# Optimization experiments

Measured on AMD Instinct MI355X. Metric: run time of the kernel, lower is better.

The kernel has to match this reference:

```python
import jax, jax.numpy as jnp
import numpy as np

N, NF, D, GH, E, B = 4096, 128, 64, 64, 32768, 32
NG, STEPS = 3, 3  # n_gcn, set2set processing steps


def setup_inputs() -> dict:
    key = jax.random.key(0)
    ks = iter(jax.random.split(key, 64))
    nrm = lambda shape: jax.random.normal(next(ks), shape, dtype=jnp.float32) * 0.05
    inp = {
        'x': jax.random.normal(next(ks), (N, NF), dtype=jnp.float32),
        'edge_attr': jax.random.uniform(next(ks), (E,), dtype=jnp.float32),
        'edge_idx': jax.random.randint(next(ks), (2, E), 0, N),
        'batch_map': jnp.sort(jax.random.randint(next(ks), (N,), 0, B)),
        # pre-GC MLP: NF->D, D->D, D->D (ReLU each)
        'pre_W0': nrm((NF, D)), 'pre_b0': nrm((D,)),
        'pre_W1': nrm((D, D)), 'pre_b1': nrm((D,)),
        'pre_W2': nrm((D, D)), 'pre_b2': nrm((D,)),
        # NNConv edge nets (stacked over NG layers): 1->GH->D*D
        'enn_W1': nrm((NG, 1, GH)), 'enn_b1': nrm((NG, GH)),
        'enn_W2': nrm((NG, GH, D * D)), 'enn_b2': nrm((NG, D * D)),
        'root_W': nrm((NG, D, D)), 'conv_b': nrm((NG, D)),
        # GRU(D, D) per layer, gate order r,z,n (torch), stored transposed for x@W
        'gru_Wih': nrm((NG, D, 3 * D)), 'gru_Whh': nrm((NG, D, 3 * D)),
        'gru_bih': nrm((NG, 3 * D)), 'gru_bhh': nrm((NG, 3 * D)),
        # Set2Set LSTM: input 2D -> hidden D, gate order i,f,g,o (torch)
        's2s_Wih': nrm((2 * D, 4 * D)), 's2s_Whh': nrm((D, 4 * D)),
        's2s_bih': nrm((4 * D,)), 's2s_bhh': nrm((4 * D,)),
        # post-GC MLP: 2D->D, D->D, D->D (ReLU each), then D->1
        'post_W0': nrm((2 * D, D)), 'post_b0': nrm((D,)),
        'post_W1': nrm((D, D)), 'post_b1': nrm((D,)),
        'post_W2': nrm((D, D)), 'post_b2': nrm((D,)),
        'post_W3': nrm((D, 1)), 'post_b3': nrm((1,)),
    }
    return inp


def _forward(x, edge_attr, pre_W0, pre_b0, pre_W1, pre_b1, pre_W2, pre_b2,
             enn_W1, enn_b1, enn_W2, enn_b2, root_W, conv_b,
             gru_Wih, gru_Whh, gru_bih, gru_bhh,
             s2s_Wih, s2s_Whh, s2s_bih, s2s_bhh,
             post_W0, post_b0, post_W1, post_b1, post_W2, post_b2,
             post_W3, post_b3, edge_idx, batch_map):
    relu, sig = jax.nn.relu, jax.nn.sigmoid
    # pre-GC layers
    out = relu(x @ pre_W0 + pre_b0)
    out = relu(out @ pre_W1 + pre_b1)
    out = relu(out @ pre_W2 + pre_b2)  # [N, D]

    src, dst = edge_idx[0], edge_idx[1]
    deg = jax.ops.segment_sum(jnp.ones((E,), out.dtype), dst, num_segments=N)
    deg = jnp.maximum(deg, 1.0)
    ea = edge_attr[:, None]  # view(-1, 1)

    for l in range(NG):
        h = out
        # NNConv: per-edge weight matrix from edge MLP
        We = relu(ea @ enn_W1[l] + enn_b1[l])              # [E, GH]
        We = (We @ enn_W2[l] + enn_b2[l]).reshape(E, D, D)  # [E, D, D]
        msg = jnp.einsum('ei,eio->eo', out[src], We)        # [E, D]
        agg = jax.ops.segment_sum(msg, dst, num_segments=N) / deg[:, None]
        conv = relu(agg + out @ root_W[l] + conv_b[l])
        # single-step GRU update (torch gate order r, z, n)
        gi = conv @ gru_Wih[l] + gru_bih[l]
        gh = h @ gru_Whh[l] + gru_bhh[l]
        i_r, i_z, i_n = jnp.split(gi, 3, axis=-1)
        h_r, h_z, h_n = jnp.split(gh, 3, axis=-1)
        r = sig(i_r + h_r)
        z = sig(i_z + h_z)
        n = jnp.tanh(i_n + r * h_n)
        out = (1.0 - z) * n + z * h

    # Set2Set pooling (early)
    q_star = jnp.zeros((B, 2 * D), out.dtype)
    hh = jnp.zeros((B, D), out.dtype)
    cc = jnp.zeros((B, D), out.dtype)
    for _ in range(STEPS):
        gates = q_star @ s2s_Wih + s2s_bih + hh @ s2s_Whh + s2s_bhh
        gi_, gf, gg, go = jnp.split(gates, 4, axis=-1)
        cc = sig(gf) * cc + sig(gi_) * jnp.tanh(gg)
        hh = sig(go) * jnp.tanh(cc)
        q = hh
        e = jnp.sum(out * q[batch_map], axis=-1)                    # [N]
        m = jax.ops.segment_max(e, batch_map, num_segments=B)
        a = jnp.exp(e - m[batch_map])
        den = jax.ops.segment_sum(a, batch_map, num_segments=B)
        a = a / den[batch_map]
        r_read = jax.ops.segment_sum(a[:, None] * out, batch_map, num_segments=B)
        q_star = jnp.concatenate([q, r_read], axis=-1)              # [B, 2D]

    # post-GC layers
    y = relu(q_star @ post_W0 + post_b0)
    y = relu(y @ post_W1 + post_b1)
    y = relu(y @ post_W2 + post_b2)
    y = y @ post_W3 + post_b3  # [B, 1]
    return y


def reference(x, edge_attr, edge_idx, batch_map, pre_W0, pre_b0, pre_W1, pre_b1,
              pre_W2, pre_b2, enn_W1, enn_b1, enn_W2, enn_b2, root_W, conv_b,
              gru_Wih, gru_Whh, gru_bih, gru_bhh, s2s_Wih, s2s_Whh, s2s_bih,
              s2s_bhh, post_W0, post_b0, post_W1, post_b1, post_W2, post_b2,
              post_W3, post_b3):
    return _forward(x, edge_attr, pre_W0, pre_b0, pre_W1, pre_b1, pre_W2, pre_b2,
                    enn_W1, enn_b1, enn_W2, enn_b2, root_W, conv_b,
                    gru_Wih, gru_Whh, gru_bih, gru_bhh,
                    s2s_Wih, s2s_Whh, s2s_bih, s2s_bhh,
                    post_W0, post_b0, post_W1, post_b1, post_W2, post_b2,
                    post_W3, post_b3, edge_idx, batch_map)
```

## Files before the change

kernel.cpp:

```cpp
#include <hip/hip_runtime.h>
#include <hip/hip_bf16.h>
#include <string.h>

#define NN   4096
#define NE   32768
#define NB   32
#define BKT  64

typedef __attribute__((ext_vector_type(8))) short short8;
typedef __attribute__((ext_vector_type(4))) float f4;

__device__ __forceinline__ float sigf(float x) { return 1.0f / (1.0f + __expf(-x)); }
__device__ __forceinline__ float bf2f(short s) {
    union { unsigned u; float f; } x;
    x.u = ((unsigned)(unsigned short)s) << 16;
    return x.f;
}
__device__ __forceinline__ short f2bf(float f) {
    __hip_bfloat16 h = __float2bfloat16(f);
    short s;
    memcpy(&s, &h, sizeof(short));
    return s;
}

__global__ __launch_bounds__(256) void k_setup(const float* __restrict__ x,
        const float* __restrict__ W0, const float* __restrict__ b0,
        const float* __restrict__ W1, const float* __restrict__ b1,
        const float* __restrict__ W2, const float* __restrict__ b2,
        const float* __restrict__ enn_W2, __hip_bfloat16* __restrict__ W2T,
        float* __restrict__ out, int* cnt_src, int* cnt_dst, int* bstart, int* bend) {
    int bid = blockIdx.x, t = threadIdx.x;
    if (bid < 32) {
        int i = bid * 256 + t;
        if (i < NN) cnt_src[i] = 0;
        else cnt_dst[i - NN] = 0;
        if (i < NB) { bstart[i] = 0x7FFFFFFF; bend[i] = 0; }
    } else if (bid < 224) {
        __shared__ __hip_bfloat16 tile[64 * 65];
        size_t base = (size_t)(bid - 32) * 4096;
        for (int i = t; i < 4096; i += 256) {
            int k = i >> 6, o = i & 63;
            tile[o * 65 + k] = __float2bfloat16(enn_W2[base + i]);
        }
        __syncthreads();
        for (int i = t; i < 4096; i += 256) {
            int o = i >> 6, k = i & 63;
            W2T[base + i] = tile[o * 65 + k];
        }
    } else {
        __shared__ float xr[4][128], ha[4][64], hb[4][64];
        int w = t >> 6, j = t & 63;
        int n = (bid - 224) * 4 + w;
        xr[w][j] = x[(size_t)n * 128 + j];
        xr[w][64 + j] = x[(size_t)n * 128 + 64 + j];
        float s = b0[j];
        #pragma unroll 8
        for (int k = 0; k < 128; ++k) s = fmaf(xr[w][k], W0[k * 64 + j], s);
        ha[w][j] = fmaxf(s, 0.f);
        s = b1[j];
        #pragma unroll 8
        for (int k = 0; k < 64; ++k) s = fmaf(ha[w][k], W1[k * 64 + j], s);
        hb[w][j] = fmaxf(s, 0.f);
        s = b2[j];
        #pragma unroll 8
        for (int k = 0; k < 64; ++k) s = fmaf(hb[w][k], W2[k * 64 + j], s);
        out[(size_t)n * 64 + j] = fmaxf(s, 0.f);
    }
}

__global__ __launch_bounds__(256) void k_gemmPbt(const float* __restrict__ out,
        const __hip_bfloat16* __restrict__ W2T_l, const float* __restrict__ b2l,
        __hip_bfloat16* __restrict__ P, float* __restrict__ BT, float* __restrict__ agg,
        const int* __restrict__ eidx, const float* __restrict__ ea,
        const int* __restrict__ bm, int* cnt_src, int* cnt_dst,
        int* csr_dst, float* csr_ea, int* bstart, int* bend) {
    int bid = blockIdx.x, t = threadIdx.x;
    if (bid < 512) {
        __shared__ __hip_bfloat16 A[64][72];
        int mtile = bid >> 3, gchunk = bid & 7;
        const float* Ain = out + (size_t)mtile * 64 * 64;
        for (int i = t; i < 4096; i += 256)
            A[i >> 6][i & 63] = __float2bfloat16(Ain[i]);
        __syncthreads();
        int wave = t >> 6, lane = t & 63;
        int laneM = lane & 15, quad = lane >> 4;
        int arow = wave * 16 + laneM;
        short8 a0 = *(const short8*)&A[arow][quad * 8];
        short8 a1 = *(const short8*)&A[arow][32 + quad * 8];
        #pragma unroll
        for (int sub = 0; sub < 4; ++sub) {
            int o0 = sub * 16;
            float accs[4][8];
            #pragma unroll
            for (int gg = 0; gg < 8; ++gg) {
                const __hip_bfloat16* Bt = W2T_l + (size_t)(gchunk * 8 + gg) * 4096;
                short8 b0v = *(const short8*)(Bt + (o0 + laneM) * 64 + quad * 8);
                short8 b1v = *(const short8*)(Bt + (o0 + laneM) * 64 + 32 + quad * 8);
                f4 acc = {0.f, 0.f, 0.f, 0.f};
                acc = __builtin_amdgcn_mfma_f32_16x16x32_bf16(a0, b0v, acc, 0, 0, 0);
                acc = __builtin_amdgcn_mfma_f32_16x16x32_bf16(a1, b1v, acc, 0, 0, 0);
                #pragma unroll
                for (int r = 0; r < 4; ++r) accs[r][gg] = acc[r];
            }
            int rowg = mtile * 64 + wave * 16 + quad * 4;
            #pragma unroll
            for (int r = 0; r < 4; ++r) {
                short8 sv;
                #pragma unroll
                for (int j = 0; j < 8; ++j)
                    sv[j] = f2bf(accs[r][j]);
                *(short8*)(P + (size_t)(rowg + r) * 4096 + gchunk * 512
                             + (o0 + laneM) * 8) = sv;
            }
        }
    } else if (bid < 1536) {
        __shared__ float sh[4][64];
        int w = t >> 6, j = t & 63;
        int n = (bid - 512) * 4 + w;
        sh[w][j] = out[(size_t)n * 64 + j];
        agg[(size_t)n * 64 + j] = 0.f;
        __syncthreads();
        float s = 0.f;
        #pragma unroll 8
        for (int k = 0; k < 64; ++k) s = fmaf(sh[w][k], b2l[k * 64 + j], s);
        BT[(size_t)n * 64 + j] = s;
    } else {
        int e = (bid - 1536) * 256 + t;
        if (e < NE) {
            int s = eidx[e];
            int d = eidx[NE + e];
            int slot = atomicAdd(&cnt_src[s], 1);
            if (slot < BKT) {
                csr_dst[s * BKT + slot] = d;
                csr_ea[s * BKT + slot] = ea[e];
            }
            atomicAdd(&cnt_dst[d], 1);
        }
        if (e < NN) {
            int b = bm[e];
            atomicMin(&bstart[b], e);
            atomicMax(&bend[b], e + 1);
        }
    }
}

#define MSG_CHUNK 32
__global__ __launch_bounds__(256, 2) void k_msg(const __hip_bfloat16* __restrict__ P,
        const float* __restrict__ BT, const int* __restrict__ cnt_src,
        const int* __restrict__ csr_dst, const float* __restrict__ csr_ea,
        const float* __restrict__ W1l, const float* __restrict__ b1l,
        float* __restrict__ agg) {
    __shared__ float wlds[4][MSG_CHUNK][64];
    int t = threadIdx.x, wave = t >> 6, lane = t & 63;
    int n = blockIdx.x * 4 + wave;
    int deg = cnt_src[n];
    if (deg > BKT) deg = BKT;
    float w1v = W1l[lane], b1v = b1l[lane];
    float preg[64];
    const __hip_bfloat16* Pn = P + (size_t)n * 4096 + lane * 8;
    #pragma unroll
    for (int c = 0; c < 8; ++c) {
        short8 v = *(const short8*)(Pn + c * 512);
        #pragma unroll
        for (int j = 0; j < 8; ++j) preg[c * 8 + j] = bf2f(v[j]);
    }
    float bt = BT[(size_t)n * 64 + lane];
    const int* bdst = csr_dst + n * BKT;
    const float* bea = csr_ea + n * BKT;
    for (int c0 = 0; c0 < deg; c0 += MSG_CHUNK) {
        int cc = deg - c0; if (cc > MSG_CHUNK) cc = MSG_CHUNK;
        for (int si = 0; si < cc; ++si) {
            float eav = bea[c0 + si];
            wlds[wave][si][lane] = fmaxf(fmaf(eav, w1v, b1v), 0.f);
        }
        for (int i = 0; i < cc; ++i) {
            int dst = bdst[c0 + i];
            const float* wr = wlds[wave][i];
            float acc0 = bt, acc1 = 0.f, acc2 = 0.f, acc3 = 0.f;
            #pragma unroll
            for (int g = 0; g < 64; g += 16) {
                float4 w0 = *(const float4*)(wr + g);
                float4 w1 = *(const float4*)(wr + g + 4);
                float4 w2 = *(const float4*)(wr + g + 8);
                float4 w3 = *(const float4*)(wr + g + 12);
                acc0 = fmaf(w0.x, preg[g], acc0);
                acc0 = fmaf(w0.y, preg[g + 1], acc0);
                acc0 = fmaf(w0.z, preg[g + 2], acc0);
                acc0 = fmaf(w0.w, preg[g + 3], acc0);
                acc1 = fmaf(w1.x, preg[g + 4], acc1);
                acc1 = fmaf(w1.y, preg[g + 5], acc1);
                acc1 = fmaf(w1.z, preg[g + 6], acc1);
                acc1 = fmaf(w1.w, preg[g + 7], acc1);
                acc2 = fmaf(w2.x, preg[g + 8], acc2);
                acc2 = fmaf(w2.y, preg[g + 9], acc2);
                acc2 = fmaf(w2.z, preg[g + 10], acc2);
                acc2 = fmaf(w2.w, preg[g + 11], acc2);
                acc3 = fmaf(w3.x, preg[g + 12], acc3);
                acc3 = fmaf(w3.y, preg[g + 13], acc3);
                acc3 = fmaf(w3.z, preg[g + 14], acc3);
                acc3 = fmaf(w3.w, preg[g + 15], acc3);
            }
            float acc = (acc0 + acc1) + (acc2 + acc3);
            atomicAdd(&agg[(size_t)dst * 64 + lane], acc);
        }
    }
}

__global__ __launch_bounds__(256) void k_gru(const float* __restrict__ out,
        const float* __restrict__ agg, const int* __restrict__ cnt_dst,
        const float* __restrict__ rootW, const float* __restrict__ convb,
        const float* __restrict__ Wih, const float* __restrict__ Whh,
        const float* __restrict__ bih, const float* __restrict__ bhh,
        float* __restrict__ outn) {
    __shared__ float sh[4][64], sc[4][64];
    int t = threadIdx.x, w = t >> 6, j = t & 63;
    int n = blockIdx.x * 4 + w;
    float hj = out[(size_t)n * 64 + j];
    sh[w][j] = hj;
    int dg = cnt_dst[n];
    float invd = 1.0f / (float)(dg > 0 ? dg : 1);
    __syncthreads();
    float s = agg[(size_t)n * 64 + j] * invd + convb[j];
    #pragma unroll 8
    for (int k = 0; k < 64; ++k) s = fmaf(sh[w][k], rootW[k * 64 + j], s);
    float conv = fmaxf(s, 0.f);
    sc[w][j] = conv;
    __syncthreads();
    float gir = bih[j], giz = bih[64 + j], gin = bih[128 + j];
    float ghr = bhh[j], ghz = bhh[64 + j], ghn = bhh[128 + j];
    #pragma unroll 4
    for (int k = 0; k < 64; ++k) {
        float c = sc[w][k], h = sh[w][k];
        gir = fmaf(c, Wih[k * 192 + j], gir);
        giz = fmaf(c, Wih[k * 192 + 64 + j], giz);
        gin = fmaf(c, Wih[k * 192 + 128 + j], gin);
        ghr = fmaf(h, Whh[k * 192 + j], ghr);
        ghz = fmaf(h, Whh[k * 192 + 64 + j], ghz);
        ghn = fmaf(h, Whh[k * 192 + 128 + j], ghn);
    }
    float r = sigf(gir + ghr);
    float z = sigf(giz + ghz);
    float nn = tanhf(gin + r * ghn);
    outn[(size_t)n * 64 + j] = (1.f - z) * nn + z * hj;
}

__global__ __launch_bounds__(1024) void k_s2s_post(const float* __restrict__ out,
        const int* __restrict__ bstart, const int* __restrict__ bend,
        const float* __restrict__ Wih, const float* __restrict__ Whh,
        const float* __restrict__ bih, const float* __restrict__ bhh,
        const float* __restrict__ pW0, const float* __restrict__ pb0,
        const float* __restrict__ pW1, const float* __restrict__ pb1,
        const float* __restrict__ pW2, const float* __restrict__ pb2,
        const float* __restrict__ pW3, const float* __restrict__ pb3,
        float* __restrict__ y) {
    __shared__ float cache[192 * 65];
    __shared__ float qs[128], hh[64], cc[64], gates[256];
    __shared__ float ebuf[1024];
    __shared__ float redbuf[1024];
    __shared__ float redw[16];
    __shared__ float smax, sinv;
    __shared__ float tmp64[64];
    int t = threadIdx.x, wave = t >> 6, lane = t & 63;
    int b = blockIdx.x;
    int s0 = bstart[b], e0 = bend[b];
    int cnt = e0 - s0;
    if (cnt < 0) cnt = 0;
    if (cnt > 1024) cnt = 1024;
    int ccnt = cnt < 192 ? cnt : 192;
    for (int li = t; li < ccnt * 64; li += 1024) {
        int rowi = li >> 6, d = li & 63;
        cache[rowi * 65 + d] = out[(size_t)(s0 + rowi) * 64 + d];
    }
    int g = t & 255, seg = t >> 8;
    const float* wp;
    int kcnt;
    if (seg == 0)      { wp = Wih + g;             kcnt = 64; }
    else if (seg == 1) { wp = Wih + 64 * 256 + g;  kcnt = 64; }
    else if (seg == 2) { wp = Whh + g;             kcnt = 32; }
    else               { wp = Whh + 32 * 256 + g;  kcnt = 32; }
    float wreg[64];
    #pragma unroll
    for (int j = 0; j < 64; ++j)
        wreg[j] = (j < kcnt) ? wp[(size_t)j * 256] : 0.f;
    if (t < 128) qs[t] = 0.f;
    if (t < 64) { hh[t] = 0.f; cc[t] = 0.f; }
    __syncthreads();
    for (int step = 0; step < 3; ++step) {
        const float* vsrc = (seg == 0) ? qs : (seg == 1) ? qs + 64
                          : (seg == 2) ? hh : hh + 32;
        float partial = 0.f;
        #pragma unroll
        for (int j = 0; j < 64; ++j)
            if (j < kcnt) partial = fmaf(vsrc[j], wreg[j], partial);
        redbuf[seg * 256 + g] = partial;
        __syncthreads();
        if (t < 256)
            gates[t] = bih[t] + bhh[t] + redbuf[t] + redbuf[256 + t]
                     + redbuf[512 + t] + redbuf[768 + t];
        __syncthreads();
        if (t < 64) {
            float cn = sigf(gates[64 + t]) * cc[t] + sigf(gates[t]) * tanhf(gates[128 + t]);
            cc[t] = cn;
            hh[t] = sigf(gates[192 + t]) * tanhf(cn);
        }
        __syncthreads();
        for (int idx = t; idx < cnt; idx += 1024) {
            float s = 0.f;
            if (idx < 192) {
                const float* row = cache + idx * 65;
                #pragma unroll 8
                for (int d = 0; d < 64; ++d) s = fmaf(row[d], hh[d], s);
            } else {
                const float* row = out + (size_t)(s0 + idx) * 64;
                for (int d = 0; d < 64; ++d) s = fmaf(row[d], hh[d], s);
            }
            ebuf[idx] = s;
        }
        __syncthreads();
        float lm = (t < cnt) ? ebuf[t] : -3.0e38f;
        #pragma unroll
        for (int off = 32; off > 0; off >>= 1) lm = fmaxf(lm, __shfl_down(lm, off, 64));
        if (lane == 0) redw[wave] = lm;
        __syncthreads();
        if (t == 0) {
            float m = redw[0];
            #pragma unroll
            for (int w2 = 1; w2 < 16; ++w2) m = fmaxf(m, redw[w2]);
            smax = m;
        }
        __syncthreads();
        float m = smax;
        float av = 0.f;
        if (t < cnt) {
            av = __expf(ebuf[t] - m);
            ebuf[t] = av;
        }
        float ls = av;
        #pragma unroll
        for (int off = 32; off > 0; off >>= 1) ls += __shfl_down(ls, off, 64);
        if (lane == 0) redw[wave] = ls;
        __syncthreads();
        if (t == 0) {
            float s = 0.f;
            #pragma unroll
            for (int w2 = 0; w2 < 16; ++w2) s += redw[w2];
            sinv = (cnt > 0) ? 1.f / s : 0.f;
        }
        __syncthreads();
        float inv = sinv;
        float r = 0.f;
        for (int idx = wave; idx < cnt; idx += 16) {
            float a = ebuf[idx];
            float v = (idx < 192) ? cache[idx * 65 + lane]
                                  : out[(size_t)(s0 + idx) * 64 + lane];
            r = fmaf(a, v, r);
        }
        redbuf[wave * 64 + lane] = r;
        __syncthreads();
        if (t < 64) {
            float s = 0.f;
            #pragma unroll
            for (int w2 = 0; w2 < 16; ++w2) s += redbuf[w2 * 64 + t];
            qs[64 + t] = s * inv;
            qs[t] = hh[t];
        }
        __syncthreads();
    }
    if (t < 64) {
        float s = pb0[t];
        #pragma unroll 4
        for (int k = 0; k < 128; ++k) s = fmaf(qs[k], pW0[k * 64 + t], s);
        tmp64[t] = fmaxf(s, 0.f);
    }
    __syncthreads();
    float h1v = 0.f;
    if (t < 64) {
        float s = pb1[t];
        #pragma unroll 4
        for (int k = 0; k < 64; ++k) s = fmaf(tmp64[k], pW1[k * 64 + t], s);
        h1v = fmaxf(s, 0.f);
    }
    __syncthreads();
    if (t < 64) tmp64[t] = h1v;
    __syncthreads();
    if (t < 64) {
        float s = pb2[t];
        #pragma unroll 4
        for (int k = 0; k < 64; ++k) s = fmaf(tmp64[k], pW2[k * 64 + t], s);
        gates[t] = fmaxf(s, 0.f) * pW3[t];
    }
    __syncthreads();
    if (t == 0) {
        float yy = pb3[0];
        for (int k = 0; k < 64; ++k) yy += gates[k];
        y[b] = yy;
    }
}


extern "C" void kernel_launch(void* const* d_in, const int* in_sizes, int n_in,
                              void* d_out, int out_size, void* d_ws, size_t ws_size,
                              hipStream_t stream) {
    const float* x         = (const float*)d_in[0];
    const float* edge_attr = (const float*)d_in[1];
    const int*   edge_idx  = (const int*)d_in[2];
    const int*   batch_map = (const int*)d_in[3];
    const float* pre_W0 = (const float*)d_in[4];
    const float* pre_b0 = (const float*)d_in[5];
    const float* pre_W1 = (const float*)d_in[6];
    const float* pre_b1 = (const float*)d_in[7];
    const float* pre_W2 = (const float*)d_in[8];
    const float* pre_b2 = (const float*)d_in[9];
    const float* enn_W1 = (const float*)d_in[10];
    const float* enn_b1 = (const float*)d_in[11];
    const float* enn_W2 = (const float*)d_in[12];
    const float* enn_b2 = (const float*)d_in[13];
    const float* root_W = (const float*)d_in[14];
    const float* conv_b = (const float*)d_in[15];
    const float* gru_Wih = (const float*)d_in[16];
    const float* gru_Whh = (const float*)d_in[17];
    const float* gru_bih = (const float*)d_in[18];
    const float* gru_bhh = (const float*)d_in[19];
    const float* s2s_Wih = (const float*)d_in[20];
    const float* s2s_Whh = (const float*)d_in[21];
    const float* s2s_bih = (const float*)d_in[22];
    const float* s2s_bhh = (const float*)d_in[23];
    const float* post_W0 = (const float*)d_in[24];
    const float* post_b0 = (const float*)d_in[25];
    const float* post_W1 = (const float*)d_in[26];
    const float* post_b1 = (const float*)d_in[27];
    const float* post_W2 = (const float*)d_in[28];
    const float* post_b2 = (const float*)d_in[29];
    const float* post_W3 = (const float*)d_in[30];
    const float* post_b3 = (const float*)d_in[31];
    float* yout = (float*)d_out;

    char* wp = (char*)d_ws;
    auto take = [&](size_t bytes) -> char* {
        char* r = wp;
        wp += (bytes + 255) & ~(size_t)255;
        return r;
    };
    float* outA = (float*)take((size_t)NN * 64 * 4);
    float* outB = (float*)take((size_t)NN * 64 * 4);
    __hip_bfloat16* P = (__hip_bfloat16*)take((size_t)NN * 4096 * 2);
    float* BT  = (float*)take((size_t)NN * 64 * 4);
    float* agg = (float*)take((size_t)NN * 64 * 4);
    __hip_bfloat16* W2T = (__hip_bfloat16*)take((size_t)3 * 64 * 4096 * 2);
    int* cnt_src  = (int*)take((size_t)NN * 4);
    int* cnt_dst  = (int*)take((size_t)NN * 4);
    int* csr_dst  = (int*)take((size_t)NN * BKT * 4);
    float* csr_ea = (float*)take((size_t)NN * BKT * 4);
    int* bstart   = (int*)take((size_t)NB * 4);
    int* bend     = (int*)take((size_t)NB * 4);

    k_setup<<<1248, 256, 0, stream>>>(x, pre_W0, pre_b0, pre_W1, pre_b1, pre_W2, pre_b2,
                                      enn_W2, W2T, outA, cnt_src, cnt_dst, bstart, bend);

    float* cur = outA;
    float* nxt = outB;
    for (int l = 0; l < 3; ++l) {
        int grid = (l == 0) ? 1664 : 1536;
        k_gemmPbt<<<grid, 256, 0, stream>>>(cur, W2T + (size_t)l * 64 * 4096,
                                            enn_b2 + (size_t)l * 4096, P, BT, agg,
                                            edge_idx, edge_attr, batch_map,
                                            cnt_src, cnt_dst, csr_dst, csr_ea,
                                            bstart, bend);
        k_msg<<<NN / 4, 256, 0, stream>>>(P, BT, cnt_src, csr_dst, csr_ea,
                                          enn_W1 + l * 64, enn_b1 + l * 64, agg);
        k_gru<<<NN / 4, 256, 0, stream>>>(cur, agg, cnt_dst, root_W + l * 4096,
                                          conv_b + l * 64, gru_Wih + l * 64 * 192,
                                          gru_Whh + l * 64 * 192, gru_bih + l * 192,
                                          gru_bhh + l * 192, nxt);
        float* tmp = cur; cur = nxt; nxt = tmp;
    }
    k_s2s_post<<<NB, 1024, 0, stream>>>(cur, bstart, bend, s2s_Wih, s2s_Whh, s2s_bih,
                                        s2s_bhh, post_W0, post_b0, post_W1, post_b1,
                                        post_W2, post_b2, post_W3, post_b3, yout);
}
```

Before: 369.1 us.

## Fuse per-node edge-net GEMM into message kernel via LDS, drop global P buffer

Folds the per-node projection GEMM (out × W2 into a 4096-wide P row) and the BT bias GEMM into the message-passing kernel. Each block computes P for 16 nodes into 128KB of LDS, using a pre-swizzled MFMA-friendly weight layout, instead of writing and re-reading a 32MB bf16 P buffer in global memory. Edge bucketing moves to a separate kernel that runs once instead of inside layer 0. The agg zeroing moves into setup and into the GRU kernel, and edge indices and attributes are loaded once per chunk and broadcast with shuffles. The trade-off is one block per CU with very large LDS, so there is less parallelism and latency hiding in the atomic-heavy message loop.

After: 372.1 us. About the same (+0.8%).

```diff
diff --git a/kernel.cpp b/kernel.cpp
--- a/kernel.cpp
+++ b/kernel.cpp
@@ -6,16 +6,12 @@
 #define NE   32768
 #define NB   32
 #define BKT  64
+#define MSG_CHUNK 16
 
 typedef __attribute__((ext_vector_type(8))) short short8;
 typedef __attribute__((ext_vector_type(4))) float f4;
 
 __device__ __forceinline__ float sigf(float x) { return 1.0f / (1.0f + __expf(-x)); }
-__device__ __forceinline__ float bf2f(short s) {
-    union { unsigned u; float f; } x;
-    x.u = ((unsigned)(unsigned short)s) << 16;
-    return x.f;
-}
 __device__ __forceinline__ short f2bf(float f) {
     __hip_bfloat16 h = __float2bfloat16(f);
     short s;
@@ -27,8 +23,9 @@
         const float* __restrict__ W0, const float* __restrict__ b0,
         const float* __restrict__ W1, const float* __restrict__ b1,
         const float* __restrict__ W2, const float* __restrict__ b2,
-        const float* __restrict__ enn_W2, __hip_bfloat16* __restrict__ W2T,
-        float* __restrict__ out, int* cnt_src, int* cnt_dst, int* bstart, int* bend) {
+        const float* __restrict__ enn_W2, __hip_bfloat16* __restrict__ W2F,
+        float* __restrict__ out, float* __restrict__ agg,
+        int* cnt_src, int* cnt_dst, int* bstart, int* bend) {
     int bid = blockIdx.x, t = threadIdx.x;
     if (bid < 32) {
         int i = bid * 256 + t;
@@ -36,23 +33,23 @@
         else cnt_dst[i - NN] = 0;
         if (i < NB) { bstart[i] = 0x7FFFFFFF; bend[i] = 0; }
     } else if (bid < 224) {
-        __shared__ __hip_bfloat16 tile[64 * 65];
+        __shared__ __hip_bfloat16 tile[4096];
         size_t base = (size_t)(bid - 32) * 4096;
         for (int i = t; i < 4096; i += 256) {
             int k = i >> 6, o = i & 63;
-            tile[o * 65 + k] = __float2bfloat16(enn_W2[base + i]);
-        }
-        __syncthreads();
-        for (int i = t; i < 4096; i += 256) {
-            int o = i >> 6, k = i & 63;
-            W2T[base + i] = tile[o * 65 + k];
-        }
+            int pos = ((o >> 4) << 10) | ((k >> 5) << 9) | (((k >> 3) & 3) << 7)
+                    | ((o & 15) << 3) | (k & 7);
+            tile[pos] = __float2bfloat16(enn_W2[base + i]);
+        }
+        __syncthreads();
+        for (int i = t; i < 4096; i += 256) W2F[base + i] = tile[i];
     } else {
         __shared__ float xr[4][128], ha[4][64], hb[4][64];
         int w = t >> 6, j = t & 63;
         int n = (bid - 224) * 4 + w;
         xr[w][j] = x[(size_t)n * 128 + j];
         xr[w][64 + j] = x[(size_t)n * 128 + 64 + j];
+        agg[(size_t)n * 64 + j] = 0.f;
         float s = b0[j];
         #pragma unroll 8
         for (int k = 0; k < 128; ++k) s = fmaf(xr[w][k], W0[k * 64 + j], s);
@@ -68,146 +65,158 @@
     }
 }
 
-__global__ __launch_bounds__(256) void k_gemmPbt(const float* __restrict__ out,
-        const __hip_bfloat16* __restrict__ W2T_l, const float* __restrict__ b2l,
-        __hip_bfloat16* __restrict__ P, float* __restrict__ BT, float* __restrict__ agg,
-        const int* __restrict__ eidx, const float* __restrict__ ea,
-        const int* __restrict__ bm, int* cnt_src, int* cnt_dst,
-        int* csr_dst, float* csr_ea, int* bstart, int* bend) {
-    int bid = blockIdx.x, t = threadIdx.x;
-    if (bid < 512) {
-        __shared__ __hip_bfloat16 A[64][72];
-        int mtile = bid >> 3, gchunk = bid & 7;
-        const float* Ain = out + (size_t)mtile * 64 * 64;
-        for (int i = t; i < 4096; i += 256)
-            A[i >> 6][i & 63] = __float2bfloat16(Ain[i]);
-        __syncthreads();
-        int wave = t >> 6, lane = t & 63;
-        int laneM = lane & 15, quad = lane >> 4;
-        int arow = wave * 16 + laneM;
-        short8 a0 = *(const short8*)&A[arow][quad * 8];
-        short8 a1 = *(const short8*)&A[arow][32 + quad * 8];
+__global__ __launch_bounds__(256) void k_bucket(const int* __restrict__ eidx,
+        const float* __restrict__ ea, const int* __restrict__ bm,
+        int* cnt_src, int* cnt_dst, int* csr_dst, float* csr_ea,
+        int* bstart, int* bend) {
+    int e = blockIdx.x * 256 + threadIdx.x;
+    if (e < NE) {
+        int s = eidx[e];
+        int d = eidx[NE + e];
+        int slot = atomicAdd(&cnt_src[s], 1);
+        if (slot < BKT) {
+            csr_dst[s * BKT + slot] = d;
+            csr_ea[s * BKT + slot] = ea[e];
+        }
+        atomicAdd(&cnt_dst[d], 1);
+    }
+    if (e < NN) {
+        int b = bm[e];
+        atomicMin(&bstart[b], e);
+        atomicMax(&bend[b], e + 1);
+    }
+}
+
+__global__ __launch_bounds__(256, 1) void k_fused(const float* __restrict__ out,
+        const __hip_bfloat16* __restrict__ W2F_l, const float* __restrict__ b2l,
+        const float* __restrict__ W1l, const float* __restrict__ b1l,
+        const int* __restrict__ cnt_src, const int* __restrict__ csr_dst,
+        const float* __restrict__ csr_ea, float* __restrict__ agg) {
+    __shared__ __hip_bfloat16 Pt[16 * 4096];
+    __shared__ float outs[16][68];
+    __shared__ float wlds[4][MSG_CHUNK][64];
+    int t = threadIdx.x, wave = t >> 6, lane = t & 63;
+    int laneM = lane & 15, quad = lane >> 4;
+    int n0 = blockIdx.x * 16;
+    for (int i = t; i < 1024; i += 256) outs[i >> 6][i & 63] = out[(size_t)n0 * 64 + i];
+    __syncthreads();
+    short8 a0, a1;
+    {
+        const float* ar = &outs[laneM][quad * 8];
+        #pragma unroll
+        for (int j = 0; j < 8; ++j) a0[j] = f2bf(ar[j]);
+        const float* ar2 = &outs[laneM][32 + quad * 8];
+        #pragma unroll
+        for (int j = 0; j < 8; ++j) a1[j] = f2bf(ar2[j]);
+    }
+    float btr[4] = {0.f, 0.f, 0.f, 0.f};
+    for (int k = 0; k < 64; ++k) {
+        float bv = b2l[k * 64 + lane];
+        #pragma unroll
+        for (int u = 0; u < 4; ++u) btr[u] = fmaf(outs[wave * 4 + u][k], bv, btr[u]);
+    }
+    #pragma unroll 2
+    for (int gp = 0; gp < 8; ++gp) {
+        int g0 = wave * 16 + gp * 2;
+        const __hip_bfloat16* BgA = W2F_l + (size_t)g0 * 4096;
+        const __hip_bfloat16* BgB = BgA + 4096;
+        int c = g0 >> 3, d = gp & 3;
+        char* wb = (char*)Pt + (quad << 15) + (c << 10) + (laneM << 4)
+                 + (((d ^ quad) & 3) << 2);
         #pragma unroll
         for (int sub = 0; sub < 4; ++sub) {
-            int o0 = sub * 16;
-            float accs[4][8];
-            #pragma unroll
-            for (int gg = 0; gg < 8; ++gg) {
-                const __hip_bfloat16* Bt = W2T_l + (size_t)(gchunk * 8 + gg) * 4096;
-                short8 b0v = *(const short8*)(Bt + (o0 + laneM) * 64 + quad * 8);
-                short8 b1v = *(const short8*)(Bt + (o0 + laneM) * 64 + 32 + quad * 8);
-                f4 acc = {0.f, 0.f, 0.f, 0.f};
-                acc = __builtin_amdgcn_mfma_f32_16x16x32_bf16(a0, b0v, acc, 0, 0, 0);
-                acc = __builtin_amdgcn_mfma_f32_16x16x32_bf16(a1, b1v, acc, 0, 0, 0);
-                #pragma unroll
-                for (int r = 0; r < 4; ++r) accs[r][gg] = acc[r];
-            }
-            int rowg = mtile * 64 + wave * 16 + quad * 4;
+            short8 bA0 = *(const short8*)(BgA + sub * 1024 + lane * 8);
+            short8 bA1 = *(const short8*)(BgA + sub * 1024 + 512 + lane * 8);
+            short8 bB0 = *(const short8*)(BgB + sub * 1024 + lane * 8);
+            short8 bB1 = *(const short8*)(BgB + sub * 1024 + 512 + lane * 8);
+            f4 accA = {0.f, 0.f, 0.f, 0.f}, accB = {0.f, 0.f, 0.f, 0.f};
+            accA = __builtin_amdgcn_mfma_f32_16x16x32_bf16(a0, bA0, accA, 0, 0, 0);
+            accA = __builtin_amdgcn_mfma_f32_16x16x32_bf16(a1, bA1, accA, 0, 0, 0);
+            accB = __builtin_amdgcn_mfma_f32_16x16x32_bf16(a0, bB0, accB, 0, 0, 0);
+            accB = __builtin_amdgcn_mfma_f32_16x16x32_bf16(a1, bB1, accB, 0, 0, 0);
+            char* wbs = wb + (sub << 8);
             #pragma unroll
             for (int r = 0; r < 4; ++r) {
-                short8 sv;
+                unsigned pk = (unsigned)(unsigned short)f2bf(accA[r])
+                            | ((unsigned)(unsigned short)f2bf(accB[r]) << 16);
+                *(unsigned*)(wbs + (r << 13)) = pk;
+            }
+        }
+    }
+    __syncthreads();
+    float w1v = W1l[lane], b1v = b1l[lane];
+    for (int u = 0; u < 4; ++u) {
+        int nloc = wave * 4 + u;
+        int n = n0 + nloc;
+        int deg = cnt_src[n];
+        if (deg > BKT) deg = BKT;
+        if (deg <= 0) continue;
+        float preg[64];
+        const char* Pn = (const char*)Pt + (nloc << 13);
+        #pragma unroll
+        for (int c = 0; c < 8; ++c) {
+            uint4 vv = *(const uint4*)(Pn + (c << 10) + (lane << 4));
+            unsigned d0 = vv.x, d1 = vv.y, d2 = vv.z, d3 = vv.w;
+            if (wave & 1) { unsigned tt = d0; d0 = d1; d1 = tt; tt = d2; d2 = d3; d3 = tt; }
+            if (wave & 2) { unsigned tt = d0; d0 = d2; d2 = tt; tt = d1; d1 = d3; d3 = tt; }
+            union { unsigned u2; float f; } cv;
+            cv.u2 = d0 << 16;          preg[c * 8 + 0] = cv.f;
+            cv.u2 = d0 & 0xFFFF0000u;  preg[c * 8 + 1] = cv.f;
+            cv.u2 = d1 << 16;          preg[c * 8 + 2] = cv.f;
+            cv.u2 = d1 & 0xFFFF0000u;  preg[c * 8 + 3] = cv.f;
+            cv.u2 = d2 << 16;          preg[c * 8 + 4] = cv.f;
+            cv.u2 = d2 & 0xFFFF0000u;  preg[c * 8 + 5] = cv.f;
+            cv.u2 = d3 << 16;          preg[c * 8 + 6] = cv.f;
+            cv.u2 = d3 & 0xFFFF0000u;  preg[c * 8 + 7] = cv.f;
+        }
+        float bt = btr[u];
+        const int* bdst = csr_dst + n * BKT;
+        const float* bea = csr_ea + n * BKT;
+        for (int c0 = 0; c0 < deg; c0 += MSG_CHUNK) {
+            int cc = deg - c0;
+            if (cc > MSG_CHUNK) cc = MSG_CHUNK;
+            int dl = 0; float el = 0.f;
+            if (lane < cc) { dl = bdst[c0 + lane]; el = bea[c0 + lane]; }
+            for (int si = 0; si < cc; ++si) {
+                float eav = __shfl(el, si, 64);
+                wlds[wave][si][lane] = fmaxf(fmaf(eav, w1v, b1v), 0.f);
+            }
+            for (int i = 0; i < cc; ++i) {
+                int dst = __shfl(dl, i, 64);
+                const float* wr = wlds[wave][i];
+                float acc0 = bt, acc1 = 0.f, acc2 = 0.f, acc3 = 0.f;
                 #pragma unroll
-                for (int j = 0; j < 8; ++j)
-                    sv[j] = f2bf(accs[r][j]);
-                *(short8*)(P + (size_t)(rowg + r) * 4096 + gchunk * 512
-                             + (o0 + laneM) * 8) = sv;
+                for (int g = 0; g < 64; g += 16) {
+                    float4 w0 = *(const float4*)(wr + g);
+                    float4 w1 = *(const float4*)(wr + g + 4);
+                    float4 w2 = *(const float4*)(wr + g + 8);
+                    float4 w3 = *(const float4*)(wr + g + 12);
+                    acc0 = fmaf(w0.x, preg[g], acc0);
+                    acc0 = fmaf(w0.y, preg[g + 1], acc0);
+                    acc0 = fmaf(w0.z, preg[g + 2], acc0);
+                    acc0 = fmaf(w0.w, preg[g + 3], acc0);
+                    acc1 = fmaf(w1.x, preg[g + 4], acc1);
+                    acc1 = fmaf(w1.y, preg[g + 5], acc1);
+                    acc1 = fmaf(w1.z, preg[g + 6], acc1);
+                    acc1 = fmaf(w1.w, preg[g + 7], acc1);
+                    acc2 = fmaf(w2.x, preg[g + 8], acc2);
+                    acc2 = fmaf(w2.y, preg[g + 9], acc2);
+                    acc2 = fmaf(w2.z, preg[g + 10], acc2);
+                    acc2 = fmaf(w2.w, preg[g + 11], acc2);
+                    acc3 = fmaf(w3.x, preg[g + 12], acc3);
+                    acc3 = fmaf(w3.y, preg[g + 13], acc3);
+                    acc3 = fmaf(w3.z, preg[g + 14], acc3);
+                    acc3 = fmaf(w3.w, preg[g + 15], acc3);
+                }
+                float acc = (acc0 + acc1) + (acc2 + acc3);
+                atomicAdd(&agg[(size_t)dst * 64 + lane], acc);
             }
         }
-    } else if (bid < 1536) {
-        __shared__ float sh[4][64];
-        int w = t >> 6, j = t & 63;
-        int n = (bid - 512) * 4 + w;
-        sh[w][j] = out[(size_t)n * 64 + j];
-        agg[(size_t)n * 64 + j] = 0.f;
-        __syncthreads();
-        float s = 0.f;
-        #pragma unroll 8
-        for (int k = 0; k < 64; ++k) s = fmaf(sh[w][k], b2l[k * 64 + j], s);
-        BT[(size_t)n * 64 + j] = s;
-    } else {
-        int e = (bid - 1536) * 256 + t;
-        if (e < NE) {
-            int s = eidx[e];
-            int d = eidx[NE + e];
-            int slot = atomicAdd(&cnt_src[s], 1);
-            if (slot < BKT) {
-                csr_dst[s * BKT + slot] = d;
-                csr_ea[s * BKT + slot] = ea[e];
-            }
-            atomicAdd(&cnt_dst[d], 1);
-        }
-        if (e < NN) {
-            int b = bm[e];
-            atomicMin(&bstart[b], e);
-            atomicMax(&bend[b], e + 1);
-        }
-    }
-}
-
-#define MSG_CHUNK 32
-__global__ __launch_bounds__(256, 2) void k_msg(const __hip_bfloat16* __restrict__ P,
-        const float* __restrict__ BT, const int* __restrict__ cnt_src,
-        const int* __restrict__ csr_dst, const float* __restrict__ csr_ea,
-        const float* __restrict__ W1l, const float* __restrict__ b1l,
-        float* __restrict__ agg) {
-    __shared__ float wlds[4][MSG_CHUNK][64];
-    int t = threadIdx.x, wave = t >> 6, lane = t & 63;
-    int n = blockIdx.x * 4 + wave;
-    int deg = cnt_src[n];
-    if (deg > BKT) deg = BKT;
-    float w1v = W1l[lane], b1v = b1l[lane];
-    float preg[64];
-    const __hip_bfloat16* Pn = P + (size_t)n * 4096 + lane * 8;
-    #pragma unroll
-    for (int c = 0; c < 8; ++c) {
-        short8 v = *(const short8*)(Pn + c * 512);
-        #pragma unroll
-        for (int j = 0; j < 8; ++j) preg[c * 8 + j] = bf2f(v[j]);
-    }
-    float bt = BT[(size_t)n * 64 + lane];
-    const int* bdst = csr_dst + n * BKT;
-    const float* bea = csr_ea + n * BKT;
-    for (int c0 = 0; c0 < deg; c0 += MSG_CHUNK) {
-        int cc = deg - c0; if (cc > MSG_CHUNK) cc = MSG_CHUNK;
-        for (int si = 0; si < cc; ++si) {
-            float eav = bea[c0 + si];
-            wlds[wave][si][lane] = fmaxf(fmaf(eav, w1v, b1v), 0.f);
-        }
-        for (int i = 0; i < cc; ++i) {
-            int dst = bdst[c0 + i];
-            const float* wr = wlds[wave][i];
-            float acc0 = bt, acc1 = 0.f, acc2 = 0.f, acc3 = 0.f;
-            #pragma unroll
-            for (int g = 0; g < 64; g += 16) {
-                float4 w0 = *(const float4*)(wr + g);
-                float4 w1 = *(const float4*)(wr + g + 4);
-                float4 w2 = *(const float4*)(wr + g + 8);
-                float4 w3 = *(const float4*)(wr + g + 12);
-                acc0 = fmaf(w0.x, preg[g], acc0);
-                acc0 = fmaf(w0.y, preg[g + 1], acc0);
-                acc0 = fmaf(w0.z, preg[g + 2], acc0);
-                acc0 = fmaf(w0.w, preg[g + 3], acc0);
-                acc1 = fmaf(w1.x, preg[g + 4], acc1);
-                acc1 = fmaf(w1.y, preg[g + 5], acc1);
-                acc1 = fmaf(w1.z, preg[g + 6], acc1);
-                acc1 = fmaf(w1.w, preg[g + 7], acc1);
-                acc2 = fmaf(w2.x, preg[g + 8], acc2);
-                acc2 = fmaf(w2.y, preg[g + 9], acc2);
-                acc2 = fmaf(w2.z, preg[g + 10], acc2);
-                acc2 = fmaf(w2.w, preg[g + 11], acc2);
-                acc3 = fmaf(w3.x, preg[g + 12], acc3);
-                acc3 = fmaf(w3.y, preg[g + 13], acc3);
-                acc3 = fmaf(w3.z, preg[g + 14], acc3);
-                acc3 = fmaf(w3.w, preg[g + 15], acc3);
-            }
-            float acc = (acc0 + acc1) + (acc2 + acc3);
-            atomicAdd(&agg[(size_t)dst * 64 + lane], acc);
-        }
     }
 }
 
 __global__ __launch_bounds__(256) void k_gru(const float* __restrict__ out,
-        const float* __restrict__ agg, const int* __restrict__ cnt_dst,
+        float* __restrict__ agg, const int* __restrict__ cnt_dst,
         const float* __restrict__ rootW, const float* __restrict__ convb,
         const float* __restrict__ Wih, const float* __restrict__ Whh,
         const float* __restrict__ bih, const float* __restrict__ bhh,
@@ -219,8 +228,10 @@
     sh[w][j] = hj;
     int dg = cnt_dst[n];
     float invd = 1.0f / (float)(dg > 0 ? dg : 1);
-    __syncthreads();
-    float s = agg[(size_t)n * 64 + j] * invd + convb[j];
+    float av = agg[(size_t)n * 64 + j];
+    agg[(size_t)n * 64 + j] = 0.f;
+    __syncthreads();
+    float s = av * invd + convb[j];
     #pragma unroll 8
     for (int k = 0; k < 64; ++k) s = fmaf(sh[w][k], rootW[k * 64 + j], s);
     float conv = fmaxf(s, 0.f);
@@ -443,10 +454,8 @@
     };
     float* outA = (float*)take((size_t)NN * 64 * 4);
     float* outB = (float*)take((size_t)NN * 64 * 4);
-    __hip_bfloat16* P = (__hip_bfloat16*)take((size_t)NN * 4096 * 2);
-    float* BT  = (float*)take((size_t)NN * 64 * 4);
-    float* agg = (float*)take((size_t)NN * 64 * 4);
-    __hip_bfloat16* W2T = (__hip_bfloat16*)take((size_t)3 * 64 * 4096 * 2);
+    float* agg  = (float*)take((size_t)NN * 64 * 4);
+    __hip_bfloat16* W2F = (__hip_bfloat16*)take((size_t)3 * 64 * 4096 * 2);
     int* cnt_src  = (int*)take((size_t)NN * 4);
     int* cnt_dst  = (int*)take((size_t)NN * 4);
     int* csr_dst  = (int*)take((size_t)NN * BKT * 4);
@@ -455,19 +464,18 @@
     int* bend     = (int*)take((size_t)NB * 4);
 
     k_setup<<<1248, 256, 0, stream>>>(x, pre_W0, pre_b0, pre_W1, pre_b1, pre_W2, pre_b2,
-                                      enn_W2, W2T, outA, cnt_src, cnt_dst, bstart, bend);
+                                      enn_W2, W2F, outA, agg, cnt_src, cnt_dst,
+                                      bstart, bend);
+    k_bucket<<<128, 256, 0, stream>>>(edge_idx, edge_attr, batch_map, cnt_src, cnt_dst,
+                                      csr_dst, csr_ea, bstart, bend);
 
     float* cur = outA;
     float* nxt = outB;
     for (int l = 0; l < 3; ++l) {
-        int grid = (l == 0) ? 1664 : 1536;
-        k_gemmPbt<<<grid, 256, 0, stream>>>(cur, W2T + (size_t)l * 64 * 4096,
-                                            enn_b2 + (size_t)l * 4096, P, BT, agg,
-                                            edge_idx, edge_attr, batch_map,
-                                            cnt_src, cnt_dst, csr_dst, csr_ea,
-                                            bstart, bend);
-        k_msg<<<NN / 4, 256, 0, stream>>>(P, BT, cnt_src, csr_dst, csr_ea,
-                                          enn_W1 + l * 64, enn_b1 + l * 64, agg);
+        k_fused<<<NN / 16, 256, 0, stream>>>(cur, W2F + (size_t)l * 64 * 4096,
+                                             enn_b2 + (size_t)l * 4096,
+                                             enn_W1 + l * 64, enn_b1 + l * 64,
+                                             cnt_src, csr_dst, csr_ea, agg);
         k_gru<<<NN / 4, 256, 0, stream>>>(cur, agg, cnt_dst, root_W + l * 4096,
                                           conv_b + l * 64, gru_Wih + l * 64 * 192,
                                           gru_Whh + l * 64 * 192, gru_bih + l * 192,
```
